# Kernel optimization log

Measured on AMD Instinct MI355X. Metric: run time of the kernel, lower is better.

Reference implementation:

```python
import jax, jax.numpy as jnp
import numpy as np

HEAD_DIM = 256
N_Q = 8
N_KV = 4
HIDDEN = 2304
WINDOW = 1024
SOFT_CAP = 50.0
MAX_WAVELENGTH = 10000.0


def _rope(x, start_index=0):
    # x: [b, s, n, h]. keras_hub RotaryEmbedding (rotate-half convention),
    # followed by Gemma's interleave permutation of the feature dim.
    b, s, n, h = x.shape
    inv_freq = 1.0 / (MAX_WAVELENGTH ** (jnp.arange(0, h, 2, dtype=jnp.float32) / h))
    pos = jnp.arange(s, dtype=jnp.float32) + start_index
    freq = pos[:, None] * inv_freq[None, :]            # [s, h/2]
    emb = jnp.concatenate([freq, freq], axis=-1)[None, :, None, :]  # [1, s, 1, h]
    cos, sin = jnp.cos(emb).astype(x.dtype), jnp.sin(emb).astype(x.dtype)
    x1, x2 = jnp.split(x, 2, axis=-1)
    rot = jnp.concatenate([-x2, x1], axis=-1)
    y = x * cos + rot * sin
    # Gemma _apply_rope: split halves then interleave (same permutation on q and k)
    a, b2 = jnp.split(y, 2, axis=-1)
    return jnp.stack([a, b2], axis=-1).reshape(x.shape)


def setup_inputs() -> dict:
    key = jax.random.key(0)
    ks = jax.random.split(key, 5)
    B, T, D = 2, 2048, HIDDEN
    x = jax.random.normal(ks[0], (B, T, D), dtype=jnp.float32)
    # causal mask [b, q_len, kv_len]
    causal = jnp.tril(jnp.ones((T, T), dtype=bool))
    attention_mask = jnp.broadcast_to(causal[None], (B, T, T))
    scale = 0.02
    Wq = jax.random.normal(ks[1], (N_Q, D, HEAD_DIM), dtype=jnp.float32) * scale
    Wk = jax.random.normal(ks[2], (N_KV, D, HEAD_DIM), dtype=jnp.float32) * scale
    Wv = jax.random.normal(ks[3], (N_KV, D, HEAD_DIM), dtype=jnp.float32) * scale
    Wo = jax.random.normal(ks[4], (N_Q, HEAD_DIM, D), dtype=jnp.float32) * scale
    return {"x": x, "attention_mask": attention_mask, "Wq": Wq, "Wk": Wk, "Wv": Wv, "Wo": Wo}


def reference(x, attention_mask, Wq, Wk, Wv, Wo):
    b, t, d = x.shape
    q = jnp.einsum('btd,ndh->btnh', x, Wq)
    k = jnp.einsum('bsd,kdh->bskh', x, Wk)
    v = jnp.einsum('bsd,kdh->bskh', x, Wv)
    q = _rope(q)
    k = _rope(k)
    s = k.shape[1]
    # sliding window band mask (triu(-w+1) & tril(w-1)), rows sliced at cache_update_index=0
    i = jnp.arange(s)[:, None]
    j = jnp.arange(s)[None, :]
    sliding = (j - i <= WINDOW - 1) & (i - j <= WINDOW - 1)
    mask = attention_mask & sliding[None, :t, :s]      # [b, t, s]
    q = q * jnp.asarray(1.0 / np.sqrt(HEAD_DIM), dtype=q.dtype)
    g = N_Q // N_KV
    qg = q.reshape(b, t, N_KV, g, HEAD_DIM)
    logits = jnp.einsum('btkgh,bskh->bkgts', qg, k).astype(jnp.float32)
    logits = jnp.tanh(logits / SOFT_CAP) * SOFT_CAP    # logit soft-cap
    m = mask[:, None, None, :, :]                      # [b, 1, 1, t, s]
    logits = jnp.where(m, logits, jnp.float32(-1e30))
    probs = jax.nn.softmax(logits, axis=-1).astype(q.dtype)
    out = jnp.einsum('bkgts,bskh->btkgh', probs, v).reshape(b, t, N_Q, HEAD_DIM)
    no_attended = jnp.all(~attention_mask, axis=-1, keepdims=True)[..., None]  # [b, t, 1, 1]
    out = jnp.where(no_attended, jnp.zeros_like(out), out)
    return jnp.einsum('btnh,nhd->btd', out, Wo)
```

## Files before the change

kernel.cpp:

```cpp
#include <hip/hip_runtime.h>
#include <math.h>

#define HEAD_DIM 256
#define N_Q 8
#define N_KV 4
#define HIDDEN 2304
#define WINDOW 1024
#define BATCH 2
#define SEQ 2048
#define BT (BATCH*SEQ)

typedef unsigned short u16;
typedef __attribute__((ext_vector_type(8))) short bf16x8;
typedef __attribute__((ext_vector_type(4))) float f32x4;

__device__ __forceinline__ u16 f2bf(float f) {
    union { float f; unsigned u; } c; c.f = f;
    unsigned r = c.u + 0x7FFF + ((c.u >> 16) & 1);
    return (u16)(r >> 16);
}
__device__ __forceinline__ float bf2f(u16 b) {
    union { float f; unsigned u; } c; c.u = ((unsigned)b) << 16;
    return c.f;
}

__global__ __launch_bounds__(256) void convert_x_kernel(
    const float* __restrict__ x, u16* __restrict__ xb, int n8)
{
    int i = blockIdx.x * 256 + threadIdx.x;
    if (i >= n8) return;
    const float4 a = ((const float4*)x)[2*i];
    const float4 b = ((const float4*)x)[2*i+1];
    u16 o[8] = { f2bf(a.x), f2bf(a.y), f2bf(a.z), f2bf(a.w),
                 f2bf(b.x), f2bf(b.y), f2bf(b.z), f2bf(b.w) };
    ((uint4*)xb)[i] = *(const uint4*)o;
}

__global__ __launch_bounds__(256) void wqkv_t_kernel(
    const float* __restrict__ Wq, const float* __restrict__ Wk,
    const float* __restrict__ Wv, u16* __restrict__ Wt)
{
    __shared__ float t[64][65];
    const int j = blockIdx.z;
    const float* W = (j < 8)  ? Wq + (size_t)j*HIDDEN*HEAD_DIM
                   : (j < 12) ? Wk + (size_t)(j-8)*HIDDEN*HEAD_DIM
                              : Wv + (size_t)(j-12)*HIDDEN*HEAD_DIM;
    const int d0 = blockIdx.x * 64, h0 = blockIdx.y * 64;
    const int tid = threadIdx.x;
    {
        const int r = tid >> 4, c4 = tid & 15;
        #pragma unroll
        for (int rr = r; rr < 64; rr += 16) {
            const float4 v = *(const float4*)(W + (size_t)(d0+rr)*HEAD_DIM + h0 + c4*4);
            t[rr][c4*4+0] = v.x; t[rr][c4*4+1] = v.y;
            t[rr][c4*4+2] = v.z; t[rr][c4*4+3] = v.w;
        }
    }
    __syncthreads();
    {
        const int hh = tid >> 2;
        #pragma unroll
        for (int it = 0; it < 2; it++) {
            const int chunk = (tid & 3) + it*4;
            u16 tmp[8];
            #pragma unroll
            for (int jj = 0; jj < 8; jj++) tmp[jj] = f2bf(t[chunk*8+jj][hh]);
            *(uint4*)&Wt[(size_t)(j*256 + h0 + hh)*HIDDEN + d0 + chunk*8] = *(const uint4*)tmp;
        }
    }
}

__global__ __launch_bounds__(256) void wo_t_kernel(
    const float* __restrict__ Wo, u16* __restrict__ Wot)
{
    __shared__ float t[64][65];
    const int k0 = blockIdx.x * 64, d0 = blockIdx.y * 64;
    const int tid = threadIdx.x;
    {
        const int r = tid >> 4, c4 = tid & 15;
        #pragma unroll
        for (int rr = r; rr < 64; rr += 16) {
            const float4 v = *(const float4*)(Wo + (size_t)(k0+rr)*HIDDEN + d0 + c4*4);
            t[rr][c4*4+0] = v.x; t[rr][c4*4+1] = v.y;
            t[rr][c4*4+2] = v.z; t[rr][c4*4+3] = v.w;
        }
    }
    __syncthreads();
    {
        const int dd = tid >> 2;
        #pragma unroll
        for (int it = 0; it < 2; it++) {
            const int chunk = (tid & 3) + it*4;
            u16 tmp[8];
            #pragma unroll
            for (int jj = 0; jj < 8; jj++) tmp[jj] = f2bf(t[chunk*8+jj][dd]);
            *(uint4*)&Wot[(size_t)(d0 + dd)*(N_Q*HEAD_DIM) + k0 + chunk*8] = *(const uint4*)tmp;
        }
    }
}

template<typename OutT>
__global__ __launch_bounds__(256) void gemm_bf16_kernel(
    const u16* __restrict__ A, const u16* __restrict__ Bt,
    OutT* __restrict__ C, int M, int N, int K)
{
    __shared__ u16 As[128*64];
    __shared__ u16 Bs[128*64];
    const int m0 = blockIdx.y * 128;
    const int n0 = blockIdx.x * 128;
    const int tid  = threadIdx.x;
    const int lane = tid & 63;
    const int wave = tid >> 6;
    const int wm = (wave & 1) * 64;
    const int wn = (wave >> 1) * 64;
    const int l16  = lane & 15;
    const int quad = lane >> 4;

    const int srow8  = lane >> 3;
    const int schunk = (lane & 7) ^ srow8;
    const u16* Ag = A  + (size_t)(m0 + wave*8 + srow8)*K + schunk*8;
    const u16* Bg = Bt + (size_t)(n0 + wave*8 + srow8)*K + schunk*8;

    const int axor = l16 & 7;
    const u16* ArA = As + (wm + l16)*64;
    const u16* BrB = Bs + (wn + l16)*64;

    f32x4 acc[4][4];
    #pragma unroll
    for (int i = 0; i < 4; i++)
        #pragma unroll
        for (int j = 0; j < 4; j++) acc[i][j] = (f32x4){0.f,0.f,0.f,0.f};

    for (int k0 = 0; k0 < K; k0 += 64) {
        __syncthreads();
        #pragma unroll
        for (int c = 0; c < 4; c++) {
            __builtin_amdgcn_global_load_lds(
                (const __attribute__((address_space(1))) unsigned int*)(Ag + (size_t)c*32*K + k0),
                (__attribute__((address_space(3))) unsigned int*)&As[(c*32 + wave*8)*64],
                16, 0, 0);
            __builtin_amdgcn_global_load_lds(
                (const __attribute__((address_space(1))) unsigned int*)(Bg + (size_t)c*32*K + k0),
                (__attribute__((address_space(3))) unsigned int*)&Bs[(c*32 + wave*8)*64],
                16, 0, 0);
        }
        __syncthreads();
        #pragma unroll
        for (int kk = 0; kk < 2; kk++) {
            bf16x8 af[4], bfr[4];
            #pragma unroll
            for (int t = 0; t < 4; t++)
                af[t]  = *(const bf16x8*)(ArA + t*16*64 + (((kk<<2)|quad) ^ axor)*8);
            #pragma unroll
            for (int t = 0; t < 4; t++)
                bfr[t] = *(const bf16x8*)(BrB + t*16*64 + (((kk<<2)|quad) ^ axor)*8);
            #pragma unroll
            for (int i = 0; i < 4; i++)
                #pragma unroll
                for (int j = 0; j < 4; j++)
                    acc[i][j] = __builtin_amdgcn_mfma_f32_16x16x32_bf16(
                                    af[i], bfr[j], acc[i][j], 0, 0, 0);
        }
    }

    #pragma unroll
    for (int i = 0; i < 4; i++) {
        const int rbase = m0 + wm + i*16 + quad*4;
        #pragma unroll
        for (int j = 0; j < 4; j++) {
            const int col = n0 + wn + j*16 + l16;
            #pragma unroll
            for (int r = 0; r < 4; r++) {
                const float v = acc[i][j][r];
                if constexpr (sizeof(OutT) == 2)
                    ((u16*)C)[(size_t)(rbase + r)*N + col] = f2bf(v);
                else
                    ((float*)C)[(size_t)(rbase + r)*N + col] = v;
            }
        }
    }
}

__global__ __launch_bounds__(256) void rope_kernel(
    const u16* __restrict__ raw, u16* __restrict__ qb, u16* __restrict__ kbf)
{
    const int r   = blockIdx.x;
    const int pos = r & (SEQ-1);
    const int tid = threadIdx.x;
    const u16* row = raw + (size_t)r * 4096;
    const float LOG1E4 = 9.210340371976184f;

    #pragma unroll
    for (int p = tid; p < 1024; p += 256) {
        const int n = p >> 7, j = p & 127;
        const float lo = bf2f(row[n*256 + j]);
        const float hi = bf2f(row[n*256 + j + 128]);
        const float inv = __expf(-LOG1E4 * (float)j * (1.0f/128.0f));
        float s, c; sincosf((float)pos * inv, &s, &c);
        qb[((size_t)r*N_Q + n)*HEAD_DIM + j]       = f2bf((lo*c - hi*s) * 0.0625f);
        qb[((size_t)r*N_Q + n)*HEAD_DIM + j + 128] = f2bf((hi*c + lo*s) * 0.0625f);
    }
    #pragma unroll
    for (int p = tid; p < 512; p += 256) {
        const int n = p >> 7, j = p & 127;
        const float lo = bf2f(row[2048 + n*256 + j]);
        const float hi = bf2f(row[2048 + n*256 + j + 128]);
        const float inv = __expf(-LOG1E4 * (float)j * (1.0f/128.0f));
        float s, c; sincosf((float)pos * inv, &s, &c);
        kbf[((size_t)r*N_KV + n)*HEAD_DIM + j]       = f2bf(lo*c - hi*s);
        kbf[((size_t)r*N_KV + n)*HEAD_DIM + j + 128] = f2bf(hi*c + lo*s);
    }
}

__global__ __launch_bounds__(256) void vtrans_kernel(
    const u16* __restrict__ raw, u16* __restrict__ vtt)
{
    __shared__ u16 T[32*264];
    const int blk = blockIdx.x;
    const int sc  = blk & 63;
    const int bk  = blk >> 6;
    const int b   = bk >> 2, kh = bk & 3;
    const int tid = threadIdx.x;

    const u16* rrow = raw + (size_t)(b*SEQ + sc*32)*4096 + 3072 + kh*256;
    {
        const int s = tid >> 3;
        #pragma unroll
        for (int it = 0; it < 4; it++) {
            const int seg = (tid & 7) + it*8;
            *(uint4*)&T[s*264 + seg*8] = *(const uint4*)(rrow + (size_t)s*4096 + seg*8);
        }
    }
    __syncthreads();
    u16* out = vtt + (size_t)blk*8192;
    #pragma unroll
    for (int it = 0; it < 4; it++) {
        const int o = tid + it*256;
        const int h = o >> 2, ss = o & 3;
        u16 tmp[8];
        #pragma unroll
        for (int j = 0; j < 8; j++) tmp[j] = T[(ss*8 + j)*264 + h];
        *(uint4*)(out + h*32 + ((ss ^ (h & 3))*8)) = *(const uint4*)tmp;
    }
}

#define AQT 64
__global__ __launch_bounds__(256) void attn_mfma_kernel(
    const u16* __restrict__ qb, const u16* __restrict__ kb,
    const u16* __restrict__ vtt, u16* __restrict__ ao)
{
    __shared__ u16 Ks[32*264];
    __shared__ u16 Vs[256*32];
    __shared__ u16 Ps[64*40];
    __shared__ float lsum[64];

    const int qh = blockIdx.y;
    const int kh = qh >> 1;
    const int bx = ((blockIdx.y >> 2) & 1) ? (gridDim.x - 1 - (int)blockIdx.x)
                                           : (int)blockIdx.x;
    const int t0 = bx * AQT;
    const int b  = t0 >> 11;
    const int tb = t0 & (SEQ-1);
    const int tid  = threadIdx.x;
    const int wave = tid >> 6;
    const int lane = tid & 63;
    const int l16  = lane & 15;
    const int quad = lane >> 4;

    bf16x8 qf[8];
    {
        const u16* qrow = qb + ((size_t)(t0 + wave*16 + l16)*N_Q + qh)*HEAD_DIM + quad*8;
        #pragma unroll
        for (int c = 0; c < 8; c++) qf[c] = *(const bf16x8*)(qrow + c*32);
    }

    f32x4 o[4][4];
    #pragma unroll
    for (int i = 0; i < 4; i++)
        #pragma unroll
        for (int j = 0; j < 4; j++) o[i][j] = (f32x4){0.f,0.f,0.f,0.f};
    float lpart[4] = {0.f, 0.f, 0.f, 0.f};

    int s_begin = tb - (WINDOW-1); if (s_begin < 0) s_begin = 0;
    const int st0 = s_begin & ~31;

    const u16* kbase = kb  + ((size_t)(b*SEQ)*N_KV + kh)*HEAD_DIM;
    const u16* vbase = vtt + ((size_t)(b*N_KV + kh)*SEQ)*HEAD_DIM;

    for (int st = st0; st < tb + AQT; st += 32) {
        __syncthreads();
        {
            const u16* vtile = vbase + (size_t)st*HEAD_DIM;
            #pragma unroll
            for (int c = 0; c < 4; c++) {
                const int off = wave*2048 + c*512;
                __builtin_amdgcn_global_load_lds(
                    (const __attribute__((address_space(1))) unsigned int*)(vtile + off + lane*8),
                    (__attribute__((address_space(3))) unsigned int*)&Vs[off],
                    16, 0, 0);
            }
            const int s = tid >> 3;
            const u16* krow = kbase + (size_t)(st + s)*(N_KV*HEAD_DIM);
            #pragma unroll
            for (int it = 0; it < 4; it++) {
                const int seg = (tid & 7) + it*8;
                *(uint4*)&Ks[s*264 + seg*8] = *(const uint4*)(krow + seg*8);
            }
        }
        __syncthreads();

        f32x4 sc[2];
        #pragma unroll
        for (int sf = 0; sf < 2; sf++) {
            f32x4 a = (f32x4){0.f,0.f,0.f,0.f};
            const u16* kr = &Ks[(sf*16 + l16)*264 + quad*8];
            #pragma unroll
            for (int c = 0; c < 8; c++)
                a = __builtin_amdgcn_mfma_f32_16x16x32_bf16(
                        qf[c], *(const bf16x8*)(kr + c*32), a, 0, 0, 0);
            sc[sf] = a;
        }

        #pragma unroll
        for (int sf = 0; sf < 2; sf++) {
            const int sg = st + sf*16 + l16;
            #pragma unroll
            for (int r = 0; r < 4; r++) {
                const int tg = tb + wave*16 + quad*4 + r;
                const float e1 = __expf(sc[sf][r] * 0.04f);
                float p = __expf(-100.0f / (e1 + 1.0f));
                const bool ok = (sg <= tg) && (tg - sg < WINDOW);
                p = ok ? p : 0.0f;
                lpart[r] += p;
                Ps[(wave*16 + quad*4 + r)*40 + sf*16 + l16] = f2bf(p);
            }
        }
        __syncthreads();

        bf16x8 ap[4];
        #pragma unroll
        for (int i = 0; i < 4; i++)
            ap[i] = *(const bf16x8*)&Ps[(i*16 + l16)*40 + quad*8];
        #pragma unroll
        for (int j = 0; j < 4; j++) {
            const int hr = wave*64 + j*16 + l16;
            const bf16x8 bv = *(const bf16x8*)&Vs[hr*32 + ((quad ^ (l16 & 3))*8)];
            #pragma unroll
            for (int i = 0; i < 4; i++)
                o[i][j] = __builtin_amdgcn_mfma_f32_16x16x32_bf16(ap[i], bv, o[i][j], 0, 0, 0);
        }
    }

    #pragma unroll
    for (int r = 0; r < 4; r++) {
        float s = lpart[r];
        #pragma unroll
        for (int sh = 1; sh <= 8; sh <<= 1) s += __shfl_xor(s, sh, 64);
        if (l16 == 0) lsum[wave*16 + quad*4 + r] = s;
    }
    __syncthreads();

    #pragma unroll
    for (int i = 0; i < 4; i++) {
        #pragma unroll
        for (int r = 0; r < 4; r++) {
            const int rl  = i*16 + quad*4 + r;
            const float inv = 1.0f / (lsum[rl] + 1e-30f);
            u16* arow = ao + ((size_t)(t0 + rl)*N_Q + qh)*HEAD_DIM + wave*64 + l16;
            #pragma unroll
            for (int j = 0; j < 4; j++)
                arow[j*16] = f2bf(o[i][j][r] * inv);
        }
    }
}

extern "C" void kernel_launch(void* const* d_in, const int* in_sizes, int n_in,
                              void* d_out, int out_size, void* d_ws, size_t ws_size,
                              hipStream_t stream)
{
    const float* x  = (const float*)d_in[0];
    const float* Wq = (const float*)d_in[2];
    const float* Wk = (const float*)d_in[3];
    const float* Wv = (const float*)d_in[4];
    const float* Wo = (const float*)d_in[5];
    float* out = (float*)d_out;

    char* w = (char*)d_ws;
    u16* qbuf = (u16*)(w);
    u16* kbuf = (u16*)(w +  16777216ull);
    u16* vtt  = (u16*)(w +  25165824ull);
    u16* aob  = (u16*)(w +  33554432ull);
    u16* xb   = (u16*)(w +  50331648ull);
    u16* wt1  = (u16*)(w +  69206016ull);
    u16* wot  = (u16*)(w +  88080384ull);
    u16* raw  = (u16*)(w +  97517568ull);

    const int n8 = BT*HIDDEN/8;
    convert_x_kernel<<<(n8+255)/256, 256, 0, stream>>>(x, xb, n8);
    wqkv_t_kernel<<<dim3(HIDDEN/64, HEAD_DIM/64, 16), 256, 0, stream>>>(Wq, Wk, Wv, wt1);
    wo_t_kernel<<<dim3(N_Q*HEAD_DIM/64, HIDDEN/64), 256, 0, stream>>>(Wo, wot);

    gemm_bf16_kernel<u16><<<dim3(4096/128, BT/128), 256, 0, stream>>>(
        xb, wt1, raw, BT, 4096, HIDDEN);
    rope_kernel<<<BT, 256, 0, stream>>>(raw, qbuf, kbuf);
    vtrans_kernel<<<BATCH*N_KV*64, 256, 0, stream>>>(raw, vtt);
    attn_mfma_kernel<<<dim3(BT/AQT, N_Q), 256, 0, stream>>>(qbuf, kbuf, vtt, aob);
    gemm_bf16_kernel<float><<<dim3(HIDDEN/128, BT/128), 256, 0, stream>>>(
        aob, wot, out, BT, HIDDEN, N_Q*HEAD_DIM);
}
```

Baseline: 408.3 us.

## Add 256x256-tile pipelined GEMM with direct-to-LDS loads for QKV projection

Adds a new 512-thread GEMM kernel that computes a 256x256 output tile per workgroup. It double-buffers LDS with global_load_lds direct copies and interleaves the prefetch of the next K-tile with MFMA work across barrier-separated phases, using s_setprio around the MFMA bursts. It also applies an XCD-aware block swizzle and an XOR-swizzled LDS layout. It replaces the 128x128 GEMM for the fused QKV projection, aiming at more data reuse per tile and at overlap of memory loads with compute. The larger tile uses a lot of LDS and registers, and with only 256 workgroups the GPU may not be fully occupied.

```diff
diff --git a/kernel.cpp b/kernel.cpp
--- a/kernel.cpp
+++ b/kernel.cpp
@@ -172,6 +172,174 @@
             #pragma unroll
             for (int r = 0; r < 4; r++) {
                 const float v = acc[i][j][r];
+                if constexpr (sizeof(OutT) == 2)
+                    ((u16*)C)[(size_t)(rbase + r)*N + col] = f2bf(v);
+                else
+                    ((float*)C)[(size_t)(rbase + r)*N + col] = v;
+            }
+        }
+    }
+}
+
+template<int KK>
+__device__ __forceinline__ void g256_ld_b(const u16* BsB, bf16x8 (&bf)[4],
+                                          int wcol, int l16, int quad, int axor)
+{
+    #pragma unroll
+    for (int j = 0; j < 4; j++)
+        bf[j] = *(const bf16x8*)(BsB + (wcol*64 + j*16 + l16)*64 + (((KK<<2)|quad)^axor)*8);
+}
+template<int MH, int KK>
+__device__ __forceinline__ void g256_ld_a(const u16* AsB, bf16x8 (&af)[4],
+                                          int wrow, int l16, int quad, int axor)
+{
+    #pragma unroll
+    for (int i = 0; i < 4; i++)
+        af[i] = *(const bf16x8*)(AsB + (wrow*128 + MH*64 + i*16 + l16)*64 + (((KK<<2)|quad)^axor)*8);
+}
+template<int MH>
+__device__ __forceinline__ void g256_mfma(const bf16x8 (&af)[4], const bf16x8 (&bf)[4],
+                                          f32x4 (&acc)[8][4])
+{
+    __builtin_amdgcn_s_setprio(1);
+    #pragma unroll
+    for (int i = 0; i < 4; i++)
+        #pragma unroll
+        for (int j = 0; j < 4; j++)
+            acc[MH*4+i][j] = __builtin_amdgcn_mfma_f32_16x16x32_bf16(
+                                 af[i], bf[j], acc[MH*4+i][j], 0, 0, 0);
+    __builtin_amdgcn_s_setprio(0);
+}
+
+template<typename OutT>
+__global__ __launch_bounds__(512, 2) void gemm256_kernel(
+    const u16* __restrict__ A, const u16* __restrict__ Bt,
+    OutT* __restrict__ C, int M, int N, int K)
+{
+    __shared__ __align__(16) u16 As[2][16384];
+    __shared__ __align__(16) u16 Bs[2][16384];
+
+    const int nwg = gridDim.x;
+    const int bid = blockIdx.x;
+    const int cpx = nwg >> 3;
+    const int swz = (bid & 7) * cpx + (bid >> 3);
+    const int NX  = N >> 8;
+    const int m0  = (swz / NX) << 8;
+    const int n0  = (swz % NX) << 8;
+
+    const int tid  = threadIdx.x;
+    const int lane = tid & 63;
+    const int wave = tid >> 6;
+    const int wrow = wave >> 2;
+    const int wcol = wave & 3;
+    const int l16  = lane & 15;
+    const int quad = lane >> 4;
+    const int axor = l16 & 7;
+
+    const int srow8  = lane >> 3;
+    const int schunk = (lane & 7) ^ srow8;
+    const u16* Ag = A  + (size_t)(m0 + wave*8 + srow8)*K + schunk*8;
+    const u16* Bg = Bt + (size_t)(n0 + wave*8 + srow8)*K + schunk*8;
+
+    u16* As0 = &As[0][0]; u16* As1 = &As[1][0];
+    u16* Bs0 = &Bs[0][0]; u16* Bs1 = &Bs[1][0];
+
+    auto STG = [&](const u16* g, u16* lds, int R0, int kt) {
+        __builtin_amdgcn_global_load_lds(
+            (const __attribute__((address_space(1))) unsigned int*)(g + (size_t)R0*K + (size_t)kt*64),
+            (__attribute__((address_space(3))) unsigned int*)(lds + (R0 + wave*8)*64),
+            16, 0, 0);
+    };
+
+    f32x4 acc[8][4];
+    #pragma unroll
+    for (int i = 0; i < 8; i++)
+        #pragma unroll
+        for (int j = 0; j < 4; j++) acc[i][j] = (f32x4){0.f,0.f,0.f,0.f};
+    bf16x8 af[4], bf[4];
+
+    #pragma unroll
+    for (int h = 0; h < 4; h++) STG(Ag, As0, h*64, 0);
+    #pragma unroll
+    for (int h = 0; h < 4; h++) STG(Bg, Bs0, h*64, 0);
+    #pragma unroll
+    for (int h = 0; h < 4; h++) STG(Ag, As1, h*64, 1);
+    #pragma unroll
+    for (int h = 0; h < 4; h++) STG(Bg, Bs1, h*64, 1);
+    asm volatile("s_waitcnt vmcnt(8)" ::: "memory");
+    __builtin_amdgcn_s_barrier();
+
+    const int NT2 = K >> 7;
+    for (int t = 0; t < NT2; ++t) {
+        const int T1 = 2*t+1, T2 = 2*t+2, T3 = 2*t+3;
+        const bool nf = (t > 0);
+        const bool nl = (t < NT2-1);
+
+        g256_ld_b<0>(Bs0, bf, wcol, l16, quad, axor);
+        g256_ld_a<0,0>(As0, af, wrow, l16, quad, axor);
+        if (nf) { STG(Bg, Bs1, 128, T1); STG(Bg, Bs1, 192, T1); }
+        __builtin_amdgcn_s_barrier();
+        g256_mfma<0>(af, bf, acc);
+        __builtin_amdgcn_s_barrier();
+
+        g256_ld_a<1,0>(As0, af, wrow, l16, quad, axor);
+        if (nf) { STG(Ag, As1, 0, T1); STG(Ag, As1, 64, T1); }
+        __builtin_amdgcn_s_barrier();
+        g256_mfma<1>(af, bf, acc);
+        __builtin_amdgcn_s_barrier();
+
+        g256_ld_b<1>(Bs0, bf, wcol, l16, quad, axor);
+        g256_ld_a<0,1>(As0, af, wrow, l16, quad, axor);
+        if (nf) { STG(Ag, As1, 128, T1); STG(Ag, As1, 192, T1); }
+        __builtin_amdgcn_s_barrier();
+        g256_mfma<0>(af, bf, acc);
+        __builtin_amdgcn_s_barrier();
+
+        g256_ld_a<1,1>(As0, af, wrow, l16, quad, axor);
+        if (nl) { STG(Bg, Bs0, 0, T2); STG(Bg, Bs0, 64, T2); }
+        __builtin_amdgcn_s_barrier();
+        g256_mfma<1>(af, bf, acc);
+        if (nl) asm volatile("s_waitcnt vmcnt(2)" ::: "memory");
+        else    asm volatile("s_waitcnt vmcnt(0)" ::: "memory");
+        __builtin_amdgcn_s_barrier();
+
+        g256_ld_b<0>(Bs1, bf, wcol, l16, quad, axor);
+        g256_ld_a<0,0>(As1, af, wrow, l16, quad, axor);
+        if (nl) { STG(Bg, Bs0, 128, T2); STG(Bg, Bs0, 192, T2); }
+        __builtin_amdgcn_s_barrier();
+        g256_mfma<0>(af, bf, acc);
+        __builtin_amdgcn_s_barrier();
+
+        g256_ld_a<1,0>(As1, af, wrow, l16, quad, axor);
+        if (nl) { STG(Ag, As0, 0, T2); STG(Ag, As0, 64, T2); }
+        __builtin_amdgcn_s_barrier();
+        g256_mfma<1>(af, bf, acc);
+        __builtin_amdgcn_s_barrier();
+
+        g256_ld_b<1>(Bs1, bf, wcol, l16, quad, axor);
+        g256_ld_a<0,1>(As1, af, wrow, l16, quad, axor);
+        if (nl) { STG(Ag, As0, 128, T2); STG(Ag, As0, 192, T2); }
+        __builtin_amdgcn_s_barrier();
+        g256_mfma<0>(af, bf, acc);
+        __builtin_amdgcn_s_barrier();
+
+        g256_ld_a<1,1>(As1, af, wrow, l16, quad, axor);
+        if (nl) { STG(Bg, Bs1, 0, T3); STG(Bg, Bs1, 64, T3); }
+        __builtin_amdgcn_s_barrier();
+        g256_mfma<1>(af, bf, acc);
+        if (nl) asm volatile("s_waitcnt vmcnt(2)" ::: "memory");
+        __builtin_amdgcn_s_barrier();
+    }
+
+    #pragma unroll
+    for (int ii = 0; ii < 8; ii++) {
+        const int rbase = m0 + wrow*128 + ii*16 + quad*4;
+        #pragma unroll
+        for (int j = 0; j < 4; j++) {
+            const int col = n0 + wcol*64 + j*16 + l16;
+            #pragma unroll
+            for (int r = 0; r < 4; r++) {
+                const float v = acc[ii][j][r];
                 if constexpr (sizeof(OutT) == 2)
                     ((u16*)C)[(size_t)(rbase + r)*N + col] = f2bf(v);
                 else
@@ -400,7 +568,7 @@
     wqkv_t_kernel<<<dim3(HIDDEN/64, HEAD_DIM/64, 16), 256, 0, stream>>>(Wq, Wk, Wv, wt1);
     wo_t_kernel<<<dim3(N_Q*HEAD_DIM/64, HIDDEN/64), 256, 0, stream>>>(Wo, wot);
 
-    gemm_bf16_kernel<u16><<<dim3(4096/128, BT/128), 256, 0, stream>>>(
+    gemm256_kernel<u16><<<(BT/256)*(4096/256), 512, 0, stream>>>(
         xb, wt1, raw, BT, 4096, HIDDEN);
     rope_kernel<<<BT, 256, 0, stream>>>(raw, qbuf, kbuf);
     vtrans_kernel<<<BATCH*N_KV*64, 256, 0, stream>>>(raw, vtt);
```

After: 393.5 us. -3.6%, faster.
